# Performance work log

Hardware: AMD Instinct MI355X
Metric: run time of the kernel (lower is better)

Reference implementation:

```python
import jax, jax.numpy as jnp
import numpy as np

B, L, D, H, NB = 8, 256, 128, 4, 2
HD = D // H
N_ITEMS, TIME_SPAN = 50000, 256
EPS = 1e-8
NEG = -(2.0 ** 32) + 1.0  # torch uses -2**32+1 padding value


def _ln(x, g, b):
    m = jnp.mean(x, -1, keepdims=True)
    v = jnp.mean((x - m) ** 2, -1, keepdims=True)
    return (x - m) / jnp.sqrt(v + EPS) * g + b


def setup_inputs() -> dict:
    ks = iter(jax.random.split(jax.random.key(0), 40))

    def nrm(shape, s=0.02):
        return jax.random.normal(next(ks), shape, jnp.float32) * s

    inp = {
        "user_ids": jax.random.randint(next(ks), (B,), 0, 1000),
        "log_seqs": jax.random.randint(next(ks), (B, L), 0, N_ITEMS + 1),
        "time_matrices": jax.random.randint(next(ks), (B, L, L), 0, TIME_SPAN + 1),
        "pos_seqs": jax.random.randint(next(ks), (B, L), 1, N_ITEMS + 1),
        "neg_seqs": jax.random.randint(next(ks), (B, L), 1, N_ITEMS + 1),
    }
    inp["item_emb"] = nrm((N_ITEMS + 1, D)).at[0].set(0.0)  # padding_idx=0
    inp["posK_emb"] = nrm((L, D))
    inp["posV_emb"] = nrm((L, D))
    inp["timeK_emb"] = nrm((TIME_SPAN + 1, D))
    inp["timeV_emb"] = nrm((TIME_SPAN + 1, D))
    inp["ln1_g"] = jnp.ones((NB, D)); inp["ln1_b"] = jnp.zeros((NB, D))
    inp["Wq"] = nrm((NB, D, D)); inp["bq"] = jnp.zeros((NB, D))
    inp["Wk"] = nrm((NB, D, D)); inp["bk"] = jnp.zeros((NB, D))
    inp["Wv"] = nrm((NB, D, D)); inp["bv"] = jnp.zeros((NB, D))
    inp["ln2_g"] = jnp.ones((NB, D)); inp["ln2_b"] = jnp.zeros((NB, D))
    inp["W1"] = nrm((NB, D, D)); inp["b1"] = jnp.zeros((NB, D))
    inp["W2"] = nrm((NB, D, D)); inp["b2"] = jnp.zeros((NB, D))
    inp["lnf_g"] = jnp.ones((D,)); inp["lnf_b"] = jnp.zeros((D,))
    return inp


def reference(user_ids, log_seqs, time_matrices, pos_seqs, neg_seqs,
              item_emb, posK_emb, posV_emb, timeK_emb, timeV_emb,
              ln1_g, ln1_b, Wq, bq, Wk, bk, Wv, bv, ln2_g, ln2_b,
              W1, b1, W2, b2, lnf_g, lnf_b):
    # dropout layers are identity in eval mode
    seqs = item_emb[log_seqs] * jnp.sqrt(jnp.float32(D))          # [B,L,D]
    tK = timeK_emb[time_matrices].reshape(B, L, L, H, HD)          # [B,Lq,Lk,H,hd]
    tV = timeV_emb[time_matrices].reshape(B, L, L, H, HD)
    pad = log_seqs == 0                                            # [B,L]
    seqs = seqs * (~pad)[..., None]
    causal = jnp.triu(jnp.ones((L, L), bool), 1)                   # ~tril -> masked
    # time_mask masks by QUERY position (matches torch unsqueeze(-1).expand)
    mask = pad[:, None, :, None] | causal[None, None]              # [B,1,Lq,Lk]
    posKh = posK_emb.reshape(L, H, HD)
    posVh = posV_emb.reshape(L, H, HD)
    for i in range(NB):
        q_in = _ln(seqs, ln1_g[i], ln1_b[i])
        Qh = (q_in @ Wq[i] + bq[i]).reshape(B, L, H, HD).transpose(0, 2, 1, 3)
        Kh = (seqs @ Wk[i] + bk[i]).reshape(B, L, H, HD).transpose(0, 2, 1, 3)
        Vh = (seqs @ Wv[i] + bv[i]).reshape(B, L, H, HD).transpose(0, 2, 1, 3)
        scores = jnp.einsum("bhqd,bhkd->bhqk", Qh, Kh)
        scores = scores + jnp.einsum("bhqd,khd->bhqk", Qh, posKh)
        scores = scores + jnp.einsum("bqkhd,bhqd->bhqk", tK, Qh)
        scores = scores / jnp.sqrt(jnp.float32(HD))
        scores = jnp.where(mask, NEG, scores)
        A = jax.nn.softmax(scores, axis=-1)                        # [B,H,Lq,Lk]
        out = jnp.einsum("bhqk,bhkd->bhqd", A, Vh)
        out = out + jnp.einsum("bhqk,khd->bhqd", A, posVh)
        out = out + jnp.einsum("bhqk,bqkhd->bhqd", A, tV)
        out = out.transpose(0, 2, 1, 3).reshape(B, L, D)
        seqs = q_in + out                                          # residual on Q
        seqs = _ln(seqs, ln2_g[i], ln2_b[i])
        h = jax.nn.relu(seqs @ W1[i] + b1[i])                      # conv1d k=1 == linear
        seqs = seqs + (h @ W2[i] + b2[i])
        seqs = seqs * (~pad)[..., None]
    feats = _ln(seqs, lnf_g, lnf_b)
    pos_logits = jnp.sum(feats * item_emb[pos_seqs], -1)           # [B,L]
    neg_logits = jnp.sum(feats * item_emb[neg_seqs], -1)
    return (pos_logits, neg_logits)
```

## Files before the change

kernel.cpp:

```cpp
#include <hip/hip_runtime.h>
#include <hip/hip_bf16.h>

#define B_ 8
#define L_ 256
#define D_ 128
#define H_ 4
#define NB_ 2
#define ROWS (B_*L_)
#define NEGV (-4294967295.0f)

typedef __hip_bfloat16 bf16;

__device__ __forceinline__ float us2f(unsigned short u){ return __uint_as_float(((unsigned)u)<<16); }
__device__ __forceinline__ unsigned short f2us(float f){ bf16 h=__float2bfloat16(f); return *(unsigned short*)&h; }
__device__ __forceinline__ float b2f(bf16 x){ return __bfloat162float(x); }

struct WPtrs { const float* p[10]; };

__global__ __launch_bounds__(256) void k_prep(const float* __restrict__ item_emb,
        const int* __restrict__ log_seqs, float* __restrict__ seqs,
        WPtrs wp, unsigned short* __restrict__ wsW,
        const float* __restrict__ timeK, const float* __restrict__ timeV,
        unsigned short* __restrict__ tmK, unsigned short* __restrict__ tmV) {
    int tid = threadIdx.x, bid = blockIdx.x;
    if (bid < 256) {
        int gi = bid*256 + tid;
        int r = gi >> 5, c4 = gi & 31;
        int id = log_seqs[r];
        float4 v = ((const float4*)item_emb)[id*32 + c4];
        float sc = (id==0) ? 0.0f : 11.3137085f;
        v.x*=sc; v.y*=sc; v.z*=sc; v.w*=sc;
        ((float4*)seqs)[gi] = v;
    } else if (bid < 416) {
        int m = (bid-256) >> 4, ch = (bid-256) & 15;
        float4 v = ((const float4*)wp.p[m])[ch*256 + tid];
        ushort4 o; o.x=f2us(v.x); o.y=f2us(v.y); o.z=f2us(v.z); o.w=f2us(v.w);
        ((ushort4*)(wsW + (size_t)m*16384))[ch*256 + tid] = o;
    } else {
        int gi = (bid-416)*256 + tid;
        if (gi < 8224) {
            float4 v = ((const float4*)timeK)[gi];
            ushort4 o; o.x=f2us(v.x); o.y=f2us(v.y); o.z=f2us(v.z); o.w=f2us(v.w);
            ((ushort4*)tmK)[gi] = o;
        } else if (gi < 16448) {
            int gj = gi - 8224;
            float4 v = ((const float4*)timeV)[gj];
            ushort4 o; o.x=f2us(v.x); o.y=f2us(v.y); o.z=f2us(v.z); o.w=f2us(v.w);
            ((ushort4*)tmV)[gj] = o;
        }
    }
}

__device__ __forceinline__ void stage_w(const unsigned short* __restrict__ Wg,
                                        unsigned short* sW, int tid){
    const uint4* src = (const uint4*)Wg;
    uint4* dst = (uint4*)sW;
    #pragma unroll
    for (int j=0;j<8;j++) dst[j*256+tid] = src[j*256+tid];
}

__device__ __forceinline__ void ln_rows(const float* sA, float* sOut,
        const float* __restrict__ g, const float* __restrict__ b,
        float* qin_out, int r0, int tid){
    int r = tid>>5, l = tid&31;
    const float* x = sA + r*128;
    float x0=x[l], x1=x[l+32], x2=x[l+64], x3=x[l+96];
    float s = x0+x1+x2+x3;
    #pragma unroll
    for (int o=16;o;o>>=1) s += __shfl_xor(s,o,64);
    float m = s*(1.f/128.f);
    float d0=x0-m,d1=x1-m,d2=x2-m,d3=x3-m;
    float v = d0*d0+d1*d1+d2*d2+d3*d3;
    #pragma unroll
    for (int o=16;o;o>>=1) v += __shfl_xor(v,o,64);
    float rstd = rsqrtf(v*(1.f/128.f)+1e-8f);
    float y0=d0*rstd*g[l]+b[l];
    float y1=d1*rstd*g[l+32]+b[l+32];
    float y2=d2*rstd*g[l+64]+b[l+64];
    float y3=d3*rstd*g[l+96]+b[l+96];
    float* o_ = sOut + r*128;
    o_[l]=y0; o_[l+32]=y1; o_[l+64]=y2; o_[l+96]=y3;
    if (qin_out){
        float* q = qin_out + (size_t)(r0+r)*128;
        q[l]=y0; q[l+32]=y1; q[l+64]=y2; q[l+96]=y3;
    }
}

__device__ __forceinline__ void gemm2x2(const float* A, const unsigned short* sW,
        int ra, int rb, int c0, float* acc){
    float a00=0,a01=0,a10=0,a11=0;
    const float* Ar = A + ra*128;
    const float* Br = A + rb*128;
    #pragma unroll 8
    for (int k=0;k<128;k++){
        ushort2 wp = *(const ushort2*)(sW + k*128 + c0);
        float w0=us2f(wp.x), w1=us2f(wp.y);
        float x0=Ar[k], x1=Br[k];
        a00=fmaf(x0,w0,a00); a01=fmaf(x0,w1,a01);
        a10=fmaf(x1,w0,a10); a11=fmaf(x1,w1,a11);
    }
    acc[0]=a00; acc[1]=a01; acc[2]=a10; acc[3]=a11;
}

__device__ __forceinline__ void gemm1x2(const float* Ar, const unsigned short* sW,
        int c0, float& o0, float& o1){
    float a0=0,a1=0;
    #pragma unroll 8
    for (int k=0;k<128;k++){
        ushort2 wp = *(const ushort2*)(sW + k*128 + c0);
        float x = Ar[k];
        a0 = fmaf(x, us2f(wp.x), a0);
        a1 = fmaf(x, us2f(wp.y), a1);
    }
    o0=a0; o1=a1;
}

__global__ __launch_bounds__(256) void k_qkv(const float* __restrict__ seqs,
        const unsigned short* __restrict__ Wqb, const unsigned short* __restrict__ Wkb,
        const unsigned short* __restrict__ Wvb,
        const float* __restrict__ bq, const float* __restrict__ bk, const float* __restrict__ bv,
        const float* __restrict__ ln1g, const float* __restrict__ ln1b,
        const float* __restrict__ posK, const float* __restrict__ posV,
        float* __restrict__ qin, bf16* __restrict__ Qo, bf16* __restrict__ Ko,
        bf16* __restrict__ Vo){
    __shared__ unsigned short sW[16384];
    __shared__ float sA[1024], sAq[1024];
    int tid = threadIdx.x;
    int m = blockIdx.x >> 8;
    int rg = blockIdx.x & 255;
    int r0 = rg*8;
    ((float4*)sA)[tid] = ((const float4*)(seqs + (size_t)r0*128))[tid];
    const unsigned short* Wg = (m==0)?Wqb:(m==1)?Wkb:Wvb;
    stage_w(Wg, sW, tid);
    __syncthreads();
    const float* src = sA;
    if (m==0){
        ln_rows(sA, sAq, ln1g, ln1b, qin, r0, tid);
        src = sAq;
        __syncthreads();
    }
    int cp = tid & 63, rp = tid >> 6;
    int c0 = 2*cp, ra = 2*rp, rb = ra+1;
    float acc[4];
    gemm2x2(src, sW, ra, rb, c0, acc);
    if (m==0){
        float b0v = bq[c0], b1v = bq[c0+1];
        ushort2 s0; s0.x=f2us(acc[0]+b0v); s0.y=f2us(acc[1]+b1v);
        ushort2 s1; s1.x=f2us(acc[2]+b0v); s1.y=f2us(acc[3]+b1v);
        *(ushort2*)((unsigned short*)Qo + (size_t)(r0+ra)*128 + c0) = s0;
        *(ushort2*)((unsigned short*)Qo + (size_t)(r0+rb)*128 + c0) = s1;
    } else {
        const float* bb = (m==1)?bk:bv;
        const float* pp = (m==1)?posK:posV;
        bf16* Oo = (m==1)?Ko:Vo;
        int qa = (r0+ra)&(L_-1), qb2 = (r0+rb)&(L_-1);
        float b0v = bb[c0], b1v = bb[c0+1];
        ushort2 s0; s0.x=f2us(acc[0]+b0v+pp[qa*128+c0]);  s0.y=f2us(acc[1]+b1v+pp[qa*128+c0+1]);
        ushort2 s1; s1.x=f2us(acc[2]+b0v+pp[qb2*128+c0]); s1.y=f2us(acc[3]+b1v+pp[qb2*128+c0+1]);
        *(ushort2*)((unsigned short*)Oo + (size_t)(r0+ra)*128 + c0) = s0;
        *(ushort2*)((unsigned short*)Oo + (size_t)(r0+rb)*128 + c0) = s1;
    }
}

__global__ __launch_bounds__(256) void k_ffn(float* __restrict__ x,
        const unsigned short* __restrict__ W1b, const unsigned short* __restrict__ W2b,
        const float* __restrict__ b1, const float* __restrict__ b2,
        const int* __restrict__ maskids){
    __shared__ unsigned short sW[16384];
    __shared__ float sA[512], sH[512];
    int tid=threadIdx.x; int r0=blockIdx.x*4;
    sA[tid]     = x[(size_t)r0*128 + tid];
    sA[tid+256] = x[(size_t)r0*128 + tid + 256];
    stage_w(W1b, sW, tid);
    __syncthreads();
    int cp=tid&63, rp=tid>>6, c0=2*cp;
    float h0,h1;
    gemm1x2(sA + rp*128, sW, c0, h0, h1);
    sH[rp*128+c0]   = fmaxf(h0+b1[c0],0.f);
    sH[rp*128+c0+1] = fmaxf(h1+b1[c0+1],0.f);
    __syncthreads();
    stage_w(W2b, sW, tid);
    __syncthreads();
    float f0,f1;
    gemm1x2(sH + rp*128, sW, c0, f0, f1);
    bool msk = maskids[r0+rp]==0;
    f0 = msk?0.f:(f0+b2[c0]  +sA[rp*128+c0]);
    f1 = msk?0.f:(f1+b2[c0+1]+sA[rp*128+c0+1]);
    x[(size_t)(r0+rp)*128 + c0]   = f0;
    x[(size_t)(r0+rp)*128 + c0+1] = f1;
}

__global__ __launch_bounds__(256) void k_lnlogits(const float* __restrict__ x,
        const float* __restrict__ lnfg, const float* __restrict__ lnfb,
        const int* __restrict__ pos_seqs, const int* __restrict__ neg_seqs,
        const float* __restrict__ item_emb, float* __restrict__ outp){
    __shared__ float sA[1024], sH[1024];
    int tid=threadIdx.x; int r0=blockIdx.x*8;
    ((float4*)sA)[tid] = ((const float4*)(x + (size_t)r0*128))[tid];
    __syncthreads();
    ln_rows(sA, sH, lnfg, lnfb, nullptr, r0, tid);
    __syncthreads();
    int w = tid>>6, lane = tid&63;
    #pragma unroll
    for (int j=0;j<4;j++){
        int o = w*4 + j;
        int row = o>>1; int neg = o&1;
        int rg = r0 + row;
        int id = neg ? neg_seqs[rg] : pos_seqs[rg];
        const float* e = item_emb + (size_t)id*128;
        const float* fr = sH + row*128;
        float s = fr[lane]*e[lane] + fr[lane+64]*e[lane+64];
        #pragma unroll
        for (int oo=32;oo;oo>>=1) s += __shfl_xor(s,oo,64);
        if (lane==0) outp[(neg?ROWS:0) + rg] = s;
    }
}

__global__ __launch_bounds__(256) void k_attn(
        const bf16* __restrict__ Q, const bf16* __restrict__ Kb,
        const bf16* __restrict__ Vb, const float* __restrict__ qin,
        const int* __restrict__ log_seqs, const int* __restrict__ tmat,
        const unsigned short* __restrict__ tmK, const unsigned short* __restrict__ tmV,
        const float* __restrict__ ln2g, const float* __restrict__ ln2b,
        float* __restrict__ outseq){
    __shared__ __align__(16) float sQ[2][D_];
    __shared__ float sS[2][H_][L_];
    __shared__ int   sTM[2][L_];
    __shared__ float sPr[2][8][D_];
    __shared__ float sRed[2][2], sRed2[2][2];
    int tid = threadIdx.x;
    int b = blockIdx.x >> 7, p = blockIdx.x & 127;
    int q1 = p, q2 = L_-1-p;
    int b0 = b*L_;
    int r1 = b0+q1, r2 = b0+q2;
    bool pad1 = log_seqs[r1]==0, pad2 = log_seqs[r2]==0;
    const float scale = 0.17677669529663687f;
    if (tid < 128) sQ[0][tid] = b2f(Q[(size_t)r1*128+tid])*scale;
    else           sQ[1][tid-128] = b2f(Q[(size_t)r2*128+(tid-128)])*scale;
    int k = tid;
    int tmv1 = tmat[(size_t)r1*L_+k], tmv2 = tmat[(size_t)r2*L_+k];
    sTM[0][k]=tmv1; sTM[1][k]=tmv2;
    __syncthreads();

    {
        const uint4* K4 = (const uint4*)(Kb + (size_t)(b0+k)*128);
        #pragma unroll
        for (int i=0;i<2;i++){
            int qq = i? q2:q1; bool pad = i? pad2:pad1;
            int tm = i? tmv2:tmv1;
            bool act = (k<=qq) && !pad;
            float acc[4] = {0.f,0.f,0.f,0.f};
            if (act){
                const uint4* T4 = (const uint4*)(tmK + (size_t)tm*128);
                const float4* Q4 = (const float4*)sQ[i];
                #pragma unroll
                for (int c=0;c<16;c++){
                    uint4 kv = K4[c];
                    uint4 tv = T4[c];
                    float4 qa = Q4[2*c], qb = Q4[2*c+1];
                    const unsigned short* ku = (const unsigned short*)&kv;
                    const unsigned short* tu = (const unsigned short*)&tv;
                    acc[c>>2] += qa.x*(us2f(ku[0])+us2f(tu[0]))
                               + qa.y*(us2f(ku[1])+us2f(tu[1]))
                               + qa.z*(us2f(ku[2])+us2f(tu[2]))
                               + qa.w*(us2f(ku[3])+us2f(tu[3]))
                               + qb.x*(us2f(ku[4])+us2f(tu[4]))
                               + qb.y*(us2f(ku[5])+us2f(tu[5]))
                               + qb.z*(us2f(ku[6])+us2f(tu[6]))
                               + qb.w*(us2f(ku[7])+us2f(tu[7]));
                }
            }
            #pragma unroll
            for (int h=0;h<H_;h++) sS[i][h][k] = act ? acc[h] : NEGV;
        }
    }
    __syncthreads();

    {
        int h = tid>>6, lane = tid&63;
        #pragma unroll
        for (int i=0;i<2;i++){
            float v0=sS[i][h][lane], v1=sS[i][h][lane+64],
                  v2=sS[i][h][lane+128], v3=sS[i][h][lane+192];
            float m = fmaxf(fmaxf(v0,v1),fmaxf(v2,v3));
            #pragma unroll
            for (int o=32;o;o>>=1) m = fmaxf(m,__shfl_xor(m,o,64));
            float e0=__expf(v0-m), e1=__expf(v1-m), e2=__expf(v2-m), e3=__expf(v3-m);
            float ss=e0+e1+e2+e3;
            #pragma unroll
            for (int o=32;o;o>>=1) ss += __shfl_xor(ss,o,64);
            float inv = 1.f/ss;
            sS[i][h][lane]=e0*inv;     sS[i][h][lane+64]=e1*inv;
            sS[i][h][lane+128]=e2*inv; sS[i][h][lane+192]=e3*inv;
        }
    }
    __syncthreads();

    {
        int dq = tid&31, slice = tid>>5, h = dq>>3;
        #pragma unroll
        for (int i=0;i<2;i++){
            int qq = i? q2:q1; bool pad = i? pad2:pad1;
            int kend = pad? L_ : qq+1;
            int k0 = slice*32;
            int kmax = kend - k0; kmax = kmax<0?0:(kmax>32?32:kmax);
            float a0=0,a1=0,a2=0,a3=0;
            for (int kk=0;kk<kmax;kk++){
                int kx = k0+kk;
                float a = sS[i][h][kx];
                int tmk = sTM[i][kx];
                ushort4 v4 = ((const ushort4*)(Vb + (size_t)(b0+kx)*128))[dq];
                ushort4 t4 = ((const ushort4*)(tmV + (size_t)tmk*128))[dq];
                a0 = fmaf(a, us2f(v4.x)+us2f(t4.x), a0);
                a1 = fmaf(a, us2f(v4.y)+us2f(t4.y), a1);
                a2 = fmaf(a, us2f(v4.z)+us2f(t4.z), a2);
                a3 = fmaf(a, us2f(v4.w)+us2f(t4.w), a3);
            }
            ((float4*)sPr[i][slice])[dq] = make_float4(a0,a1,a2,a3);
        }
    }
    __syncthreads();

    {
        int i = tid>>7, l = tid&127;
        int rr = i? r2:r1;
        float v = qin[(size_t)rr*128 + l];
        #pragma unroll
        for (int sl=0;sl<8;sl++) v += sPr[i][sl][l];
        float s = v;
        #pragma unroll
        for (int o=32;o;o>>=1) s += __shfl_xor(s,o,64);
        if ((tid&63)==0) sRed[i][(tid>>6)&1] = s;
        __syncthreads();
        float m = (sRed[i][0]+sRed[i][1])*(1.f/128.f);
        float d = v-m;
        float vv = d*d;
        #pragma unroll
        for (int o=32;o;o>>=1) vv += __shfl_xor(vv,o,64);
        if ((tid&63)==0) sRed2[i][(tid>>6)&1] = vv;
        __syncthreads();
        float rstd = rsqrtf((sRed2[i][0]+sRed2[i][1])*(1.f/128.f)+1e-8f);
        outseq[(size_t)rr*128+l] = d*rstd*ln2g[l]+ln2b[l];
    }
}

extern "C" void kernel_launch(void* const* d_in, const int* in_sizes, int n_in,
                              void* d_out, int out_size, void* d_ws, size_t ws_size,
                              hipStream_t stream) {
    const int* log_seqs = (const int*)d_in[1];
    const int* tmat     = (const int*)d_in[2];
    const int* pos_seqs = (const int*)d_in[3];
    const int* neg_seqs = (const int*)d_in[4];
    const float* item_emb = (const float*)d_in[5];
    const float* posK  = (const float*)d_in[6];
    const float* posV  = (const float*)d_in[7];
    const float* timeK = (const float*)d_in[8];
    const float* timeV = (const float*)d_in[9];
    const float* ln1_g = (const float*)d_in[10];
    const float* ln1_b = (const float*)d_in[11];
    const float* Wq = (const float*)d_in[12];
    const float* bqv = (const float*)d_in[13];
    const float* Wk = (const float*)d_in[14];
    const float* bk = (const float*)d_in[15];
    const float* Wv = (const float*)d_in[16];
    const float* bv = (const float*)d_in[17];
    const float* ln2_g = (const float*)d_in[18];
    const float* ln2_b = (const float*)d_in[19];
    const float* W1 = (const float*)d_in[20];
    const float* b1 = (const float*)d_in[21];
    const float* W2 = (const float*)d_in[22];
    const float* b2 = (const float*)d_in[23];
    const float* lnf_g = (const float*)d_in[24];
    const float* lnf_b = (const float*)d_in[25];

    const int NE = ROWS * D_;
    char* wsb = (char*)d_ws;
    float* s_seqs = (float*)(wsb + 0);
    float* s_qin  = (float*)(wsb + (size_t)NE * 4);
    bf16*  s_Q    = (bf16*) (wsb + (size_t)NE * 8);
    bf16*  s_K    = (bf16*) (wsb + (size_t)NE * 8 + (size_t)NE * 2);
    bf16*  s_V    = (bf16*) (wsb + (size_t)NE * 8 + (size_t)NE * 4);
    unsigned short* wsW = (unsigned short*)(wsb + (size_t)NE * 14);
    unsigned short* tmK = (unsigned short*)(wsb + (size_t)NE * 14 + 327680);
    unsigned short* tmV = tmK + 32896;

    const int DD = D_*D_;
    WPtrs wp;
    wp.p[0]=Wq;      wp.p[1]=Wk;      wp.p[2]=Wv;      wp.p[3]=W1;      wp.p[4]=W2;
    wp.p[5]=Wq+DD;   wp.p[6]=Wk+DD;   wp.p[7]=Wv+DD;   wp.p[8]=W1+DD;   wp.p[9]=W2+DD;

    k_prep<<<482, 256, 0, stream>>>(item_emb, log_seqs, s_seqs, wp, wsW,
                                    timeK, timeV, tmK, tmV);
    for (int i = 0; i < NB_; i++) {
        k_qkv<<<768, 256, 0, stream>>>(s_seqs, wsW+(5*i+0)*DD, wsW+(5*i+1)*DD, wsW+(5*i+2)*DD,
                bqv+i*D_, bk+i*D_, bv+i*D_, ln1_g+i*D_, ln1_b+i*D_, posK, posV,
                s_qin, s_Q, s_K, s_V);
        k_attn<<<1024, 256, 0, stream>>>(s_Q, s_K, s_V, s_qin, log_seqs, tmat,
                tmK, tmV, ln2_g+i*D_, ln2_b+i*D_, s_seqs);
        k_ffn<<<512, 256, 0, stream>>>(s_seqs, wsW+(5*i+3)*DD, wsW+(5*i+4)*DD,
                b1+i*D_, b2+i*D_, log_seqs);
    }
    k_lnlogits<<<256, 256, 0, stream>>>(s_seqs, lnf_g, lnf_b, pos_seqs, neg_seqs,
                                        item_emb, (float*)d_out);
}
```

Measured before the change: 218.9 us.

## Precompute Q·timeK table and bucket attention weights by time for timeV

```diff
diff --git a/kernel.cpp b/kernel.cpp
--- a/kernel.cpp
+++ b/kernel.cpp
@@ -8,6 +8,8 @@
 #define NB_ 2
 #define ROWS (B_*L_)
 #define NEGV (-4294967295.0f)
+#define TSTRIDE 260
+#define RSTRIDE (H_*TSTRIDE)
 
 typedef __hip_bfloat16 bf16;
 
@@ -162,57 +164,28 @@
     }
 }
 
-__global__ __launch_bounds__(256) void k_ffn(float* __restrict__ x,
-        const unsigned short* __restrict__ W1b, const unsigned short* __restrict__ W2b,
-        const float* __restrict__ b1, const float* __restrict__ b2,
-        const int* __restrict__ maskids){
-    __shared__ unsigned short sW[16384];
-    __shared__ float sA[512], sH[512];
-    int tid=threadIdx.x; int r0=blockIdx.x*4;
-    sA[tid]     = x[(size_t)r0*128 + tid];
-    sA[tid+256] = x[(size_t)r0*128 + tid + 256];
-    stage_w(W1b, sW, tid);
-    __syncthreads();
-    int cp=tid&63, rp=tid>>6, c0=2*cp;
-    float h0,h1;
-    gemm1x2(sA + rp*128, sW, c0, h0, h1);
-    sH[rp*128+c0]   = fmaxf(h0+b1[c0],0.f);
-    sH[rp*128+c0+1] = fmaxf(h1+b1[c0+1],0.f);
-    __syncthreads();
-    stage_w(W2b, sW, tid);
-    __syncthreads();
-    float f0,f1;
-    gemm1x2(sH + rp*128, sW, c0, f0, f1);
-    bool msk = maskids[r0+rp]==0;
-    f0 = msk?0.f:(f0+b2[c0]  +sA[rp*128+c0]);
-    f1 = msk?0.f:(f1+b2[c0+1]+sA[rp*128+c0+1]);
-    x[(size_t)(r0+rp)*128 + c0]   = f0;
-    x[(size_t)(r0+rp)*128 + c0+1] = f1;
-}
-
-__global__ __launch_bounds__(256) void k_lnlogits(const float* __restrict__ x,
-        const float* __restrict__ lnfg, const float* __restrict__ lnfb,
-        const int* __restrict__ pos_seqs, const int* __restrict__ neg_seqs,
-        const float* __restrict__ item_emb, float* __restrict__ outp){
-    __shared__ float sA[1024], sH[1024];
-    int tid=threadIdx.x; int r0=blockIdx.x*8;
-    ((float4*)sA)[tid] = ((const float4*)(x + (size_t)r0*128))[tid];
-    __syncthreads();
-    ln_rows(sA, sH, lnfg, lnfb, nullptr, r0, tid);
-    __syncthreads();
-    int w = tid>>6, lane = tid&63;
-    #pragma unroll
-    for (int j=0;j<4;j++){
-        int o = w*4 + j;
-        int row = o>>1; int neg = o&1;
-        int rg = r0 + row;
-        int id = neg ? neg_seqs[rg] : pos_seqs[rg];
-        const float* e = item_emb + (size_t)id*128;
-        const float* fr = sH + row*128;
-        float s = fr[lane]*e[lane] + fr[lane+64]*e[lane+64];
-        #pragma unroll
-        for (int oo=32;oo;oo>>=1) s += __shfl_xor(s,oo,64);
-        if (lane==0) outp[(neg?ROWS:0) + rg] = s;
+__global__ __launch_bounds__(256) void k_dqt(const bf16* __restrict__ Q,
+        const unsigned short* __restrict__ tmK, float* __restrict__ DQT){
+    __shared__ float sq[128];
+    int tid = threadIdx.x, bq = blockIdx.x;
+    if (tid < 128) sq[tid] = b2f(Q[(size_t)bq*128+tid]) * 0.17677669529663687f;
+    __syncthreads();
+    for (int t = tid; t < 257; t += 256){
+        const uint4* T4 = (const uint4*)(tmK + (size_t)t*128);
+        float acc[4] = {0.f,0.f,0.f,0.f};
+        #pragma unroll
+        for (int c=0;c<16;c++){
+            uint4 tv = T4[c];
+            const unsigned short* tu = (const unsigned short*)&tv;
+            const float* qq = sq + c*8;
+            acc[c>>2] += qq[0]*us2f(tu[0]) + qq[1]*us2f(tu[1])
+                       + qq[2]*us2f(tu[2]) + qq[3]*us2f(tu[3])
+                       + qq[4]*us2f(tu[4]) + qq[5]*us2f(tu[5])
+                       + qq[6]*us2f(tu[6]) + qq[7]*us2f(tu[7]);
+        }
+        #pragma unroll
+        for (int h=0;h<H_;h++)
+            DQT[(size_t)bq*RSTRIDE + h*TSTRIDE + t] = acc[h];
     }
 }
 
@@ -220,14 +193,14 @@
         const bf16* __restrict__ Q, const bf16* __restrict__ Kb,
         const bf16* __restrict__ Vb, const float* __restrict__ qin,
         const int* __restrict__ log_seqs, const int* __restrict__ tmat,
-        const unsigned short* __restrict__ tmK, const unsigned short* __restrict__ tmV,
-        const float* __restrict__ ln2g, const float* __restrict__ ln2b,
-        float* __restrict__ outseq){
+        const float* __restrict__ DQT, float* __restrict__ Wout,
+        float* __restrict__ pre){
     __shared__ __align__(16) float sQ[2][D_];
     __shared__ float sS[2][H_][L_];
     __shared__ int   sTM[2][L_];
     __shared__ float sPr[2][8][D_];
-    __shared__ float sRed[2][2], sRed2[2][2];
+    __shared__ float sDQ[2][H_][TSTRIDE];
+    __shared__ float sWH[2][H_][TSTRIDE];
     int tid = threadIdx.x;
     int b = blockIdx.x >> 7, p = blockIdx.x & 127;
     int q1 = p, q2 = L_-1-p;
@@ -240,6 +213,13 @@
     int k = tid;
     int tmv1 = tmat[(size_t)r1*L_+k], tmv2 = tmat[(size_t)r2*L_+k];
     sTM[0][k]=tmv1; sTM[1][k]=tmv2;
+    float* sDQf = (float*)sDQ; float* sWHf = (float*)sWH;
+    for (int j=tid; j<2*RSTRIDE; j+=256){
+        int i = j >= RSTRIDE;
+        int rest = j - i*RSTRIDE;
+        sDQf[j] = DQT[(size_t)(i? r2:r1)*RSTRIDE + rest];
+        sWHf[j] = 0.f;
+    }
     __syncthreads();
 
     {
@@ -251,27 +231,21 @@
             bool act = (k<=qq) && !pad;
             float acc[4] = {0.f,0.f,0.f,0.f};
             if (act){
-                const uint4* T4 = (const uint4*)(tmK + (size_t)tm*128);
                 const float4* Q4 = (const float4*)sQ[i];
                 #pragma unroll
                 for (int c=0;c<16;c++){
                     uint4 kv = K4[c];
-                    uint4 tv = T4[c];
                     float4 qa = Q4[2*c], qb = Q4[2*c+1];
                     const unsigned short* ku = (const unsigned short*)&kv;
-                    const unsigned short* tu = (const unsigned short*)&tv;
-                    acc[c>>2] += qa.x*(us2f(ku[0])+us2f(tu[0]))
-                               + qa.y*(us2f(ku[1])+us2f(tu[1]))
-                               + qa.z*(us2f(ku[2])+us2f(tu[2]))
-                               + qa.w*(us2f(ku[3])+us2f(tu[3]))
-                               + qb.x*(us2f(ku[4])+us2f(tu[4]))
-                               + qb.y*(us2f(ku[5])+us2f(tu[5]))
-                               + qb.z*(us2f(ku[6])+us2f(tu[6]))
-                               + qb.w*(us2f(ku[7])+us2f(tu[7]));
+                    acc[c>>2] += qa.x*us2f(ku[0]) + qa.y*us2f(ku[1])
+                               + qa.z*us2f(ku[2]) + qa.w*us2f(ku[3])
+                               + qb.x*us2f(ku[4]) + qb.y*us2f(ku[5])
+                               + qb.z*us2f(ku[6]) + qb.w*us2f(ku[7]);
                 }
             }
             #pragma unroll
-            for (int h=0;h<H_;h++) sS[i][h][k] = act ? acc[h] : NEGV;
+            for (int h=0;h<H_;h++)
+                sS[i][h][k] = act ? acc[h] + sDQ[i][h][tm] : NEGV;
         }
     }
     __syncthreads();
@@ -296,6 +270,13 @@
     }
     __syncthreads();
 
+    #pragma unroll
+    for (int i=0;i<2;i++){
+        int tm = i? tmv2:tmv1;
+        #pragma unroll
+        for (int h=0;h<H_;h++) atomicAdd(&sWH[i][h][tm], sS[i][h][k]);
+    }
+
     {
         int dq = tid&31, slice = tid>>5, h = dq>>3;
         #pragma unroll
@@ -308,13 +289,11 @@
             for (int kk=0;kk<kmax;kk++){
                 int kx = k0+kk;
                 float a = sS[i][h][kx];
-                int tmk = sTM[i][kx];
                 ushort4 v4 = ((const ushort4*)(Vb + (size_t)(b0+kx)*128))[dq];
-                ushort4 t4 = ((const ushort4*)(tmV + (size_t)tmk*128))[dq];
-                a0 = fmaf(a, us2f(v4.x)+us2f(t4.x), a0);
-                a1 = fmaf(a, us2f(v4.y)+us2f(t4.y), a1);
-                a2 = fmaf(a, us2f(v4.z)+us2f(t4.z), a2);
-                a3 = fmaf(a, us2f(v4.w)+us2f(t4.w), a3);
+                a0 = fmaf(a, us2f(v4.x), a0);
+                a1 = fmaf(a, us2f(v4.y), a1);
+                a2 = fmaf(a, us2f(v4.z), a2);
+                a3 = fmaf(a, us2f(v4.w), a3);
             }
             ((float4*)sPr[i][slice])[dq] = make_float4(a0,a1,a2,a3);
         }
@@ -327,20 +306,94 @@
         float v = qin[(size_t)rr*128 + l];
         #pragma unroll
         for (int sl=0;sl<8;sl++) v += sPr[i][sl][l];
-        float s = v;
+        pre[(size_t)rr*128+l] = v;
+    }
+    for (int j=tid; j<2*RSTRIDE; j+=256){
+        int i = j >= RSTRIDE;
+        int rest = j - i*RSTRIDE;
+        Wout[(size_t)(i? r2:r1)*RSTRIDE + rest] = sWHf[j];
+    }
+}
+
+__global__ __launch_bounds__(256) void k_tvffn(const float* __restrict__ pre,
+        const float* __restrict__ Wt, const unsigned short* __restrict__ tmV,
+        const unsigned short* __restrict__ W1b, const unsigned short* __restrict__ W2b,
+        const float* __restrict__ b1, const float* __restrict__ b2,
+        const int* __restrict__ maskids,
+        const float* __restrict__ ln2g, const float* __restrict__ ln2b,
+        float* __restrict__ outseq){
+    __shared__ unsigned short sW[16384];
+    __shared__ float sA[512], sH[512];
+    int tid=threadIdx.x; int r0=blockIdx.x*4;
+    int rp=tid>>6, l=tid&63, c0=2*l, h=c0>>5;
+    int r = r0+rp;
+    stage_w(W1b, sW, tid);
+    float o0 = pre[(size_t)r*128+c0], o1 = pre[(size_t)r*128+c0+1];
+    {
+        const float* Wr = Wt + (size_t)r*RSTRIDE + h*TSTRIDE;
+        const unsigned short* tv = tmV + c0;
+        for (int t=0;t<257;t++){
+            float w = Wr[t];
+            if (w != 0.f){
+                ushort2 vv = *(const ushort2*)(tv + (size_t)t*128);
+                o0 = fmaf(w, us2f(vv.x), o0);
+                o1 = fmaf(w, us2f(vv.y), o1);
+            }
+        }
+    }
+    {
+        float s = o0+o1;
         #pragma unroll
         for (int o=32;o;o>>=1) s += __shfl_xor(s,o,64);
-        if ((tid&63)==0) sRed[i][(tid>>6)&1] = s;
-        __syncthreads();
-        float m = (sRed[i][0]+sRed[i][1])*(1.f/128.f);
-        float d = v-m;
-        float vv = d*d;
-        #pragma unroll
-        for (int o=32;o;o>>=1) vv += __shfl_xor(vv,o,64);
-        if ((tid&63)==0) sRed2[i][(tid>>6)&1] = vv;
-        __syncthreads();
-        float rstd = rsqrtf((sRed2[i][0]+sRed2[i][1])*(1.f/128.f)+1e-8f);
-        outseq[(size_t)rr*128+l] = d*rstd*ln2g[l]+ln2b[l];
+        float m = s*(1.f/128.f);
+        float d0=o0-m, d1=o1-m;
+        float v = d0*d0+d1*d1;
+        #pragma unroll
+        for (int o=32;o;o>>=1) v += __shfl_xor(v,o,64);
+        float rstd = rsqrtf(v*(1.f/128.f)+1e-8f);
+        sA[rp*128+c0]   = d0*rstd*ln2g[c0]+ln2b[c0];
+        sA[rp*128+c0+1] = d1*rstd*ln2g[c0+1]+ln2b[c0+1];
+    }
+    __syncthreads();
+    float h0,h1;
+    gemm1x2(sA + rp*128, sW, c0, h0, h1);
+    sH[rp*128+c0]   = fmaxf(h0+b1[c0],0.f);
+    sH[rp*128+c0+1] = fmaxf(h1+b1[c0+1],0.f);
+    __syncthreads();
+    stage_w(W2b, sW, tid);
+    __syncthreads();
+    float f0,f1;
+    gemm1x2(sH + rp*128, sW, c0, f0, f1);
+    bool msk = maskids[r]==0;
+    f0 = msk?0.f:(f0+b2[c0]  +sA[rp*128+c0]);
+    f1 = msk?0.f:(f1+b2[c0+1]+sA[rp*128+c0+1]);
+    outseq[(size_t)r*128 + c0]   = f0;
+    outseq[(size_t)r*128 + c0+1] = f1;
+}
+
+__global__ __launch_bounds__(256) void k_lnlogits(const float* __restrict__ x,
+        const float* __restrict__ lnfg, const float* __restrict__ lnfb,
+        const int* __restrict__ pos_seqs, const int* __restrict__ neg_seqs,
+        const float* __restrict__ item_emb, float* __restrict__ outp){
+    __shared__ float sA[1024], sH[1024];
+    int tid=threadIdx.x; int r0=blockIdx.x*8;
+    ((float4*)sA)[tid] = ((const float4*)(x + (size_t)r0*128))[tid];
+    __syncthreads();
+    ln_rows(sA, sH, lnfg, lnfb, nullptr, r0, tid);
+    __syncthreads();
+    int w = tid>>6, lane = tid&63;
+    #pragma unroll
+    for (int j=0;j<4;j++){
+        int o = w*4 + j;
+        int row = o>>1; int neg = o&1;
+        int rg = r0 + row;
+        int id = neg ? neg_seqs[rg] : pos_seqs[rg];
+        const float* e = item_emb + (size_t)id*128;
+        const float* fr = sH + row*128;
+        float s = fr[lane]*e[lane] + fr[lane+64]*e[lane+64];
+        #pragma unroll
+        for (int oo=32;oo;oo>>=1) s += __shfl_xor(s,oo,64);
+        if (lane==0) outp[(neg?ROWS:0) + rg] = s;
     }
 }
 
@@ -383,6 +436,9 @@
     unsigned short* wsW = (unsigned short*)(wsb + (size_t)NE * 14);
     unsigned short* tmK = (unsigned short*)(wsb + (size_t)NE * 14 + 327680);
     unsigned short* tmV = tmK + 32896;
+    float* s_pre  = (float*)(wsb + (16u<<20));
+    float* s_DQT  = (float*)(wsb + (20u<<20));
+    float* s_W    = (float*)(wsb + (32u<<20));
 
     const int DD = D_*D_;
     WPtrs wp;
@@ -395,10 +451,12 @@
         k_qkv<<<768, 256, 0, stream>>>(s_seqs, wsW+(5*i+0)*DD, wsW+(5*i+1)*DD, wsW+(5*i+2)*DD,
                 bqv+i*D_, bk+i*D_, bv+i*D_, ln1_g+i*D_, ln1_b+i*D_, posK, posV,
                 s_qin, s_Q, s_K, s_V);
+        k_dqt<<<2048, 256, 0, stream>>>(s_Q, tmK, s_DQT);
         k_attn<<<1024, 256, 0, stream>>>(s_Q, s_K, s_V, s_qin, log_seqs, tmat,
-                tmK, tmV, ln2_g+i*D_, ln2_b+i*D_, s_seqs);
-        k_ffn<<<512, 256, 0, stream>>>(s_seqs, wsW+(5*i+3)*DD, wsW+(5*i+4)*DD,
-                b1+i*D_, b2+i*D_, log_seqs);
+                s_DQT, s_W, s_pre);
+        k_tvffn<<<512, 256, 0, stream>>>(s_pre, s_W, tmV,
+                wsW+(5*i+3)*DD, wsW+(5*i+4)*DD, b1+i*D_, b2+i*D_, log_seqs,
+                ln2_g+i*D_, ln2_b+i*D_, s_seqs);
     }
     k_lnlogits<<<256, 256, 0, stream>>>(s_seqs, lnf_g, lnf_b, pos_seqs, neg_seqs,
                                         item_emb, (float*)d_out);
```

Measured after the change: 373.0 us. +70.4%, slower.
